# Performance work log

Hardware: AMD Instinct MI355X
Metric: run time of the kernel (lower is better)

## Reference

```python
import jax, jax.numpy as jnp
import numpy as np

NNZ = 16777216  # 2**24 nonzeros
D = 2048        # dense size (D, D, D); sum over dim 2 -> (D, D)


def setup_inputs() -> dict:
    key = jax.random.key(0)
    kv, ki = jax.random.split(key)
    values = jax.random.normal(kv, (NNZ,), dtype=jnp.float32)
    indices = jax.random.randint(ki, (3, NNZ), 0, D, dtype=jnp.int64)
    return {"values": values, "indices": indices}


def reference(values, indices):
    # sparse_coo_tensor(indices, values, size=(D,D,D)) -> sparse.sum(dim=2) -> to_dense()
    # is equivalent to a scatter-add of values keyed by (indices[0], indices[1]):
    # the third index only distinguishes entries that get summed away, and COO
    # coalescing already sums duplicate coordinates.
    out = jnp.zeros((D, D), dtype=jnp.float32)
    out = out.at[indices[0], indices[1]].add(values)
    return out
```

## Files before the change

### kernel.cpp

```cpp
#include <hip/hip_runtime.h>

#define NNZ 16777216
#define D 2048
#define NB 256
#define ROWS_PER_B 8
#define R 16
#define CAPR 4864u
#define CAPT (R * CAPR)
#define K1_BLOCK 512
#define K1_EPT 16
#define K1_CHUNK (K1_BLOCK * K1_EPT)
#define K1_VEC (K1_EPT / 4)
#define K2_BLOCK 512

__global__ __launch_bounds__(K1_BLOCK) void bin_scatter(
    const float* __restrict__ values,
    const int* __restrict__ idx0,
    const int* __restrict__ idx1,
    unsigned int* __restrict__ bins,
    unsigned int* __restrict__ cursor)
{
    __shared__ unsigned int lhist[NB];
    __shared__ unsigned int sprefix[NB];
    __shared__ unsigned int sgbase[NB];
    __shared__ unsigned int wsum[4];
    __shared__ unsigned int skey[K1_CHUNK];
    __shared__ unsigned short sval[K1_CHUNK];

    const int tid = threadIdx.x;
    const unsigned int r = (unsigned int)blockIdx.x & (R - 1);
    if (tid < NB) lhist[tid] = 0;
    __syncthreads();

    const int vecBase = blockIdx.x * (K1_CHUNK / 4);

    float4 v[K1_VEC]; int4 a[K1_VEC]; int4 c[K1_VEC];
#pragma unroll
    for (int it = 0; it < K1_VEC; ++it) {
        int g = vecBase + it * K1_BLOCK + tid;
        v[it] = reinterpret_cast<const float4*>(values)[g];
        a[it] = reinterpret_cast<const int4*>(idx0)[g];
        c[it] = reinterpret_cast<const int4*>(idx1)[g];
    }

    unsigned short rank[K1_EPT];
#pragma unroll
    for (int it = 0; it < K1_VEC; ++it) {
        const int* ap = reinterpret_cast<const int*>(&a[it]);
#pragma unroll
        for (int e = 0; e < 4; ++e)
            rank[it * 4 + e] = (unsigned short)atomicAdd(&lhist[ap[e] >> 3], 1u);
    }
    __syncthreads();

    unsigned int x = 0, cnt = 0;
    if (tid < NB) {
        const int lane = tid & 63;
        cnt = lhist[tid];
        x = cnt;
#pragma unroll
        for (int dlt = 1; dlt < 64; dlt <<= 1) {
            unsigned int y = __shfl_up(x, dlt, 64);
            if (lane >= dlt) x += y;
        }
        if (lane == 63) wsum[tid >> 6] = x;
        sgbase[tid] = cnt ? atomicAdd(&cursor[r * NB + tid], cnt) : 0u;
    }
    __syncthreads();
    if (tid < NB) {
        const int wid = tid >> 6;
        unsigned int off = 0;
#pragma unroll
        for (int wjj = 0; wjj < 4; ++wjj) off += (wjj < wid) ? wsum[wjj] : 0u;
        sprefix[tid] = x - cnt + off;
    }
    __syncthreads();

#pragma unroll
    for (int it = 0; it < K1_VEC; ++it) {
        const int*   ap = reinterpret_cast<const int*>(&a[it]);
        const int*   cp = reinterpret_cast<const int*>(&c[it]);
        const float* vp = reinterpret_cast<const float*>(&v[it]);
#pragma unroll
        for (int e = 0; e < 4; ++e) {
            int i0 = ap[e], i1 = cp[e];
            unsigned int slot = sprefix[i0 >> 3] + rank[it * 4 + e];
            unsigned int fb = __float_as_uint(vp[e]);
            skey[slot] = ((unsigned int)i0 << 11) | (unsigned int)i1;
            sval[slot] = (unsigned short)((fb + 0x7fffu + ((fb >> 16) & 1u)) >> 16);
        }
    }
    __syncthreads();

#pragma unroll
    for (int it = 0; it < K1_EPT; ++it) {
        int s = it * K1_BLOCK + tid;
        unsigned int k = skey[s];
        unsigned int b = k >> 14;
        unsigned int rel = sgbase[b] + ((unsigned int)s - sprefix[b]);
        if (rel < CAPR)
            bins[b * CAPT + r * CAPR + rel] = ((k & 0x3FFFu) << 16) | (unsigned int)sval[s];
    }
}

__global__ __launch_bounds__(K2_BLOCK) void bucket_accumulate(
    const unsigned int* __restrict__ bins,
    const unsigned int* __restrict__ cursor,
    float* __restrict__ out)
{
    __shared__ float tile[ROWS_PER_B * D];

    const int b = blockIdx.x;
    const int tid = threadIdx.x;

    for (int j = tid; j < ROWS_PER_B * D / 4; j += K2_BLOCK)
        reinterpret_cast<float4*>(tile)[j] = make_float4(0.f, 0.f, 0.f, 0.f);
    __syncthreads();

    unsigned int n[R];
#pragma unroll
    for (int rr = 0; rr < R; ++rr) {
        unsigned int t = cursor[rr * NB + b];
        n[rr] = t > CAPR ? CAPR : t;
    }

    const uint4* b4 = reinterpret_cast<const uint4*>(bins);
    uint4 p[R];
    unsigned int msk = 0;
#pragma unroll
    for (int rr = 0; rr < R; ++rr) {
        unsigned int nv = n[rr] >> 2;
        unsigned int seg4 = (unsigned int)b * (CAPT / 4) + (unsigned int)rr * (CAPR / 4);
        if ((unsigned int)tid < nv) { p[rr] = b4[seg4 + tid]; msk |= 1u << rr; }
    }
#pragma unroll
    for (int rr = 0; rr < R; ++rr) {
        if (msk & (1u << rr)) {
            atomicAdd(&tile[p[rr].x >> 16], __uint_as_float(p[rr].x << 16));
            atomicAdd(&tile[p[rr].y >> 16], __uint_as_float(p[rr].y << 16));
            atomicAdd(&tile[p[rr].z >> 16], __uint_as_float(p[rr].z << 16));
            atomicAdd(&tile[p[rr].w >> 16], __uint_as_float(p[rr].w << 16));
        }
    }

#pragma unroll
    for (int rr = 0; rr < R; ++rr) {
        unsigned int nv = n[rr] >> 2;
        unsigned int seg4 = (unsigned int)b * (CAPT / 4) + (unsigned int)rr * (CAPR / 4);
        for (unsigned int i = (unsigned int)tid + K2_BLOCK; i < nv; i += K2_BLOCK) {
            uint4 q = b4[seg4 + i];
            atomicAdd(&tile[q.x >> 16], __uint_as_float(q.x << 16));
            atomicAdd(&tile[q.y >> 16], __uint_as_float(q.y << 16));
            atomicAdd(&tile[q.z >> 16], __uint_as_float(q.z << 16));
            atomicAdd(&tile[q.w >> 16], __uint_as_float(q.w << 16));
        }
        unsigned int rem = n[rr] & 3u;
        if ((unsigned int)tid < rem) {
            unsigned int w = bins[(seg4 << 2) + (nv << 2) + tid];
            atomicAdd(&tile[w >> 16], __uint_as_float(w << 16));
        }
    }
    __syncthreads();

    float4* o4 = reinterpret_cast<float4*>(out + (size_t)b * ROWS_PER_B * D);
    for (int j = tid; j < ROWS_PER_B * D / 4; j += K2_BLOCK)
        o4[j] = reinterpret_cast<float4*>(tile)[j];
}

__global__ __launch_bounds__(256) void scatter_add_kernel(
    const float* __restrict__ values,
    const int* __restrict__ idx0,
    const int* __restrict__ idx1,
    float* __restrict__ out)
{
    const int nvec = NNZ / 4;
    int tid = blockIdx.x * blockDim.x + threadIdx.x;
    int stride = gridDim.x * blockDim.x;
    for (int i = tid; i < nvec; i += stride) {
        const float4 v = reinterpret_cast<const float4*>(values)[i];
        const int4   a = reinterpret_cast<const int4*>(idx0)[i];
        const int4   b = reinterpret_cast<const int4*>(idx1)[i];
        atomicAdd(&out[a.x * D + b.x], v.x);
        atomicAdd(&out[a.y * D + b.y], v.y);
        atomicAdd(&out[a.z * D + b.z], v.z);
        atomicAdd(&out[a.w * D + b.w], v.w);
    }
}

extern "C" void kernel_launch(void* const* d_in, const int* in_sizes, int n_in,
                              void* d_out, int out_size, void* d_ws, size_t ws_size,
                              hipStream_t stream) {
    const float* values  = (const float*)d_in[0];
    const int*   indices = (const int*)d_in[1];
    const int*   idx0 = indices;
    const int*   idx1 = indices + NNZ;
    float* out = (float*)d_out;

    const size_t cur_bytes = (size_t)R * NB * sizeof(unsigned int);
    const size_t need = cur_bytes + (size_t)NB * CAPT * sizeof(unsigned int);

    if (ws_size < need) {
        hipMemsetAsync(out, 0, (size_t)out_size * sizeof(float), stream);
        const int nvec = NNZ / 4;
        scatter_add_kernel<<<(nvec + 255) / 256, 256, 0, stream>>>(values, idx0, idx1, out);
        return;
    }

    unsigned int* cursor = (unsigned int*)d_ws;
    unsigned int* bins   = (unsigned int*)((char*)d_ws + cur_bytes);

    hipMemsetAsync(cursor, 0, cur_bytes, stream);
    bin_scatter<<<NNZ / K1_CHUNK, K1_BLOCK, 0, stream>>>(values, idx0, idx1, bins, cursor);
    bucket_accumulate<<<NB, K2_BLOCK, 0, stream>>>(bins, cursor, out);
}
```

Baseline: 154.7 us.

## Pad per-bucket segments to 32-entry multiples for aligned full-line bin writes

Each block rounds every bucket's count up to a multiple of 32 and fills the padding slots in shared memory with zero-valued entries, so its global bin writes form aligned, fully used 128-byte chunks. The per-region capacity grows to absorb the padding, and the accumulate kernel skips zero words and drops the remainder tail handling. This trades more bytes written and read, a larger workspace and a serial padding loop for better write coalescing. Zero-valued true entries are skipped as well, which is harmless since adding zero changes nothing.

```diff
diff --git a/kernel.cpp b/kernel.cpp
--- a/kernel.cpp
+++ b/kernel.cpp
@@ -5,12 +5,13 @@
 #define NB 256
 #define ROWS_PER_B 8
 #define R 16
-#define CAPR 4864u
+#define CAPR 8192u
 #define CAPT (R * CAPR)
 #define K1_BLOCK 512
 #define K1_EPT 16
 #define K1_CHUNK (K1_BLOCK * K1_EPT)
 #define K1_VEC (K1_EPT / 4)
+#define PSEG 16384
 #define K2_BLOCK 512
 
 __global__ __launch_bounds__(K1_BLOCK) void bin_scatter(
@@ -21,11 +22,13 @@
     unsigned int* __restrict__ cursor)
 {
     __shared__ unsigned int lhist[NB];
-    __shared__ unsigned int sprefix[NB];
+    __shared__ unsigned int ppref[NB];
     __shared__ unsigned int sgbase[NB];
+    __shared__ unsigned int scnt[NB];
     __shared__ unsigned int wsum[4];
-    __shared__ unsigned int skey[K1_CHUNK];
-    __shared__ unsigned short sval[K1_CHUNK];
+    __shared__ unsigned int stotal;
+    __shared__ unsigned int skey[PSEG];
+    __shared__ unsigned short sval[PSEG];
 
     const int tid = threadIdx.x;
     const unsigned int r = (unsigned int)blockIdx.x & (R - 1);
@@ -53,18 +56,20 @@
     }
     __syncthreads();
 
-    unsigned int x = 0, cnt = 0;
+    unsigned int x = 0, pcnt = 0, cnt = 0;
     if (tid < NB) {
         const int lane = tid & 63;
         cnt = lhist[tid];
-        x = cnt;
+        pcnt = (cnt + 31u) & ~31u;
+        x = pcnt;
 #pragma unroll
         for (int dlt = 1; dlt < 64; dlt <<= 1) {
             unsigned int y = __shfl_up(x, dlt, 64);
             if (lane >= dlt) x += y;
         }
         if (lane == 63) wsum[tid >> 6] = x;
-        sgbase[tid] = cnt ? atomicAdd(&cursor[r * NB + tid], cnt) : 0u;
+        sgbase[tid] = pcnt ? atomicAdd(&cursor[r * NB + tid], pcnt) : 0u;
+        scnt[tid] = cnt;
     }
     __syncthreads();
     if (tid < NB) {
@@ -72,7 +77,8 @@
         unsigned int off = 0;
 #pragma unroll
         for (int wjj = 0; wjj < 4; ++wjj) off += (wjj < wid) ? wsum[wjj] : 0u;
-        sprefix[tid] = x - cnt + off;
+        ppref[tid] = x - pcnt + off;
+        if (tid == NB - 1) stotal = x + off;
     }
     __syncthreads();
 
@@ -84,20 +90,27 @@
 #pragma unroll
         for (int e = 0; e < 4; ++e) {
             int i0 = ap[e], i1 = cp[e];
-            unsigned int slot = sprefix[i0 >> 3] + rank[it * 4 + e];
+            unsigned int slot = ppref[i0 >> 3] + rank[it * 4 + e];
             unsigned int fb = __float_as_uint(vp[e]);
             skey[slot] = ((unsigned int)i0 << 11) | (unsigned int)i1;
             sval[slot] = (unsigned short)((fb + 0x7fffu + ((fb >> 16) & 1u)) >> 16);
         }
     }
-    __syncthreads();
-
-#pragma unroll
-    for (int it = 0; it < K1_EPT; ++it) {
-        int s = it * K1_BLOCK + tid;
+    if (tid < NB) {
+        unsigned int base = ppref[tid];
+        unsigned int pc = (scnt[tid] + 31u) & ~31u;
+        for (unsigned int j = scnt[tid]; j < pc; ++j) {
+            skey[base + j] = (unsigned int)tid << 14;
+            sval[base + j] = 0;
+        }
+    }
+    __syncthreads();
+
+    const unsigned int total = stotal;
+    for (unsigned int s = tid; s < total; s += K1_BLOCK) {
         unsigned int k = skey[s];
         unsigned int b = k >> 14;
-        unsigned int rel = sgbase[b] + ((unsigned int)s - sprefix[b]);
+        unsigned int rel = sgbase[b] + (s - ppref[b]);
         if (rel < CAPR)
             bins[b * CAPT + r * CAPR + rel] = ((k & 0x3FFFu) << 16) | (unsigned int)sval[s];
     }
@@ -124,6 +137,8 @@
         n[rr] = t > CAPR ? CAPR : t;
     }
 
+#define DOW(w) if (w) atomicAdd(&tile[(w) >> 16], __uint_as_float((w) << 16));
+
     const uint4* b4 = reinterpret_cast<const uint4*>(bins);
     uint4 p[R];
     unsigned int msk = 0;
@@ -136,10 +151,7 @@
 #pragma unroll
     for (int rr = 0; rr < R; ++rr) {
         if (msk & (1u << rr)) {
-            atomicAdd(&tile[p[rr].x >> 16], __uint_as_float(p[rr].x << 16));
-            atomicAdd(&tile[p[rr].y >> 16], __uint_as_float(p[rr].y << 16));
-            atomicAdd(&tile[p[rr].z >> 16], __uint_as_float(p[rr].z << 16));
-            atomicAdd(&tile[p[rr].w >> 16], __uint_as_float(p[rr].w << 16));
+            DOW(p[rr].x) DOW(p[rr].y) DOW(p[rr].z) DOW(p[rr].w)
         }
     }
 
@@ -149,17 +161,10 @@
         unsigned int seg4 = (unsigned int)b * (CAPT / 4) + (unsigned int)rr * (CAPR / 4);
         for (unsigned int i = (unsigned int)tid + K2_BLOCK; i < nv; i += K2_BLOCK) {
             uint4 q = b4[seg4 + i];
-            atomicAdd(&tile[q.x >> 16], __uint_as_float(q.x << 16));
-            atomicAdd(&tile[q.y >> 16], __uint_as_float(q.y << 16));
-            atomicAdd(&tile[q.z >> 16], __uint_as_float(q.z << 16));
-            atomicAdd(&tile[q.w >> 16], __uint_as_float(q.w << 16));
-        }
-        unsigned int rem = n[rr] & 3u;
-        if ((unsigned int)tid < rem) {
-            unsigned int w = bins[(seg4 << 2) + (nv << 2) + tid];
-            atomicAdd(&tile[w >> 16], __uint_as_float(w << 16));
-        }
-    }
+            DOW(q.x) DOW(q.y) DOW(q.z) DOW(q.w)
+        }
+    }
+#undef DOW
     __syncthreads();
 
     float4* o4 = reinterpret_cast<float4*>(out + (size_t)b * ROWS_PER_B * D);
```

Result: slower. 206.2 us (+33.3%).
